# Kernel tuning notes

Measured on AMD Instinct MI355X. Metric: run time of the kernel, lower is better.

## Reference

```python
import jax, jax.numpy as jnp
import numpy as np

BN_EPS = 1e-5
SG = jax.lax.stop_gradient


def _silu(z):
    return z * jax.nn.sigmoid(z)


def _binary_activation(x):
    # forward value = sign(x); backward goes through piecewise quadratic out3 (STE)
    out1 = jnp.where(x < -1, -1.0, x * x + 2 * x)
    out2 = jnp.where(x < 0, out1, -x * x + 2 * x)
    out3 = jnp.where(x < 1, out2, 1.0)
    return SG(jnp.sign(x)) - SG(out3) + out3


def _binarize_weight(w):
    # per-output-channel scaling factor * sign(w), STE through clipped weights
    sf = SG(jnp.mean(jnp.abs(w), axis=(1, 2, 3), keepdims=True))  # [O,1,1,1]
    cw = jnp.clip(w, -1.0, 1.0)
    return SG(sf * jnp.sign(w)) - SG(cw) + cw


def _conv3x3_s2(x, w, b):
    y = jax.lax.conv_general_dilated(
        x, w, window_strides=(2, 2), padding=((1, 1), (1, 1)),
        dimension_numbers=("NCHW", "OIHW", "NCHW"))
    return y + b[None, :, None, None]


def _batchnorm_train(x, gamma, beta):
    # training-mode BN: batch statistics over (N,H,W), biased variance
    mean = jnp.mean(x, axis=(0, 2, 3), keepdims=True)
    var = jnp.mean((x - mean) ** 2, axis=(0, 2, 3), keepdims=True)
    xhat = (x - mean) * jax.lax.rsqrt(var + BN_EPS)
    return xhat * gamma[None, :, None, None] + beta[None, :, None, None]


def _learnable_bias(x, emb, w, b):
    # bias = zero_module(linear)(SiLU(emb)) broadcast over H,W
    bias = _silu(emb) @ w.T + b  # [B, C]
    return x + bias[:, :, None, None]


def _avgpool2(x):
    B, C, H, W = x.shape
    return x.reshape(B, C, H // 2, 2, W // 2, 2).mean(axis=(3, 5))


def setup_inputs() -> dict:
    key = jax.random.key(0)
    ks = jax.random.split(key, 16)
    B, Cin, P, E, H, W = 32, 128, 256, 512, 64, 64
    scalor = P // Cin  # 2
    inp = {
        "x": jax.random.normal(ks[0], (B, Cin, H, W), jnp.float32),
        "emb": jax.random.normal(ks[1], (B, E), jnp.float32),
        "m1_w": jax.random.normal(ks[2], (Cin, E), jnp.float32) * 0.02,
        "m1_b": jnp.zeros((Cin,), jnp.float32),
        "conv_w": jax.random.uniform(ks[3], (scalor, Cin, Cin, 3, 3), jnp.float32, -1.0, 1.0) * 0.1,
        "conv_b": jax.random.normal(ks[4], (scalor, Cin), jnp.float32) * 0.01,
        "bn_g": jnp.ones((scalor, Cin), jnp.float32),
        "bn_b": jnp.zeros((scalor, Cin), jnp.float32),
        "m2_w": jax.random.normal(ks[5], (P, E), jnp.float32) * 0.02,
        "m2_b": jnp.zeros((P,), jnp.float32),
        "prelu_a": jnp.full((P,), 0.25, jnp.float32),
        "m3_w": jax.random.normal(ks[6], (P, E), jnp.float32) * 0.02,
        "m3_b": jnp.zeros((P,), jnp.float32),
    }
    return inp


def reference(x, emb, m1_w, m1_b, conv_w, conv_b, bn_g, bn_b,
              m2_w, m2_b, prelu_a, m3_w, m3_b):
    scalor = conv_w.shape[0]
    out = _learnable_bias(x, emb, m1_w, m1_b)
    out = _binary_activation(out)
    xp = _avgpool2(x)  # residual, [B,Cin,H/2,W/2]
    out_list = []
    for i in range(scalor):
        bw = _binarize_weight(conv_w[i])
        y = _conv3x3_s2(out, bw, conv_b[i])
        y = _batchnorm_train(y, bn_g[i], bn_b[i])
        out_list.append(y + xp)
    o = jnp.concatenate(out_list, axis=1)  # [B, planes, H/2, W/2]
    o = _learnable_bias(o, emb, m2_w, m2_b)
    a = prelu_a[None, :, None, None]
    o = jnp.where(o > 0, o, a * o)  # PReLU per channel
    o = _learnable_bias(o, emb, m3_w, m3_b)
    return o
```

## Files before the change

### kernel.cpp

```cpp
#include <hip/hip_runtime.h>
#include <cstdint>
#include <cstddef>

#define B_  32
#define CIN 128
#define P_  256
#define E_  512
#define H_  64
#define W_  64
#define HO  32
#define WO  32

#define APITCH 65
#define APIX   4225

__global__ void k_bw(const float* __restrict__ emb,
                     const float* __restrict__ m1_w, const float* __restrict__ m1_b,
                     const float* __restrict__ m2_w, const float* __restrict__ m2_b,
                     const float* __restrict__ m3_w, const float* __restrict__ m3_b,
                     const float* __restrict__ conv_w,
                     float* __restrict__ b1, float* __restrict__ b2, float* __restrict__ b3,
                     float* __restrict__ sf, unsigned int* __restrict__ wbits,
                     int* __restrict__ cwrow, int* __restrict__ cwcol, int* __restrict__ cw0,
                     float* __restrict__ s1, float* __restrict__ s2) {
    int bid = blockIdx.x;
    int tid = threadIdx.x;
    int wave = tid >> 6, lane = tid & 63;

    if (bid < B_ * 160) {
        int n = bid / 160, rg = bid % 160;
        int row = rg * 4 + wave;
        const float* sp = emb + n * E_;
        const float* wrow; float bias; float* dst;
        if (row < CIN)            { wrow = m1_w + (size_t)row * E_;          bias = m1_b[row]; dst = b1 + n * CIN + row; }
        else if (row < CIN + P_)  { int c = row - CIN;      wrow = m2_w + (size_t)c * E_; bias = m2_b[c]; dst = b2 + n * P_ + c; }
        else                      { int c = row - CIN - P_; wrow = m3_w + (size_t)c * E_; bias = m3_b[c]; dst = b3 + n * P_ + c; }
        float acc = 0.f;
        #pragma unroll
        for (int j = 0; j < 8; j++) {
            int k = j * 64 + lane;
            float e = sp[k];
            acc += (e / (1.f + expf(-e))) * wrow[k];
        }
        #pragma unroll
        for (int off = 32; off > 0; off >>= 1) acc += __shfl_down(acc, off);
        if (lane == 0) *dst = acc + bias;
        return;
    }

    int base = (bid - B_ * 160) * 2;
    int oc = base + (wave >> 1);
    int iw = wave & 1;
    int i  = iw * 64 + lane;
    if (lane == 0 && iw == 0) { s1[oc] = 0.f; s2[oc] = 0.f; }
    const float* wp = conv_w + ((size_t)oc * CIN + i) * 9;
    float w[9]; float s = 0.f;
    int pc[9];
    #pragma unroll
    for (int t = 0; t < 9; t++) { w[t] = wp[t]; s += fabsf(w[t]); }
    #pragma unroll
    for (int t = 0; t < 9; t++) {
        unsigned long long m = __ballot(w[t] < 0.f);
        pc[t] = __popcll(m);
        if (lane == 0) {
            wbits[oc * 36 + t * 4 + iw * 2 + 0] = (unsigned int)(m & 0xffffffffull);
            wbits[oc * 36 + t * 4 + iw * 2 + 1] = (unsigned int)(m >> 32);
        }
    }
    #pragma unroll
    for (int off = 32; off > 0; off >>= 1) s += __shfl_down(s, off);
    __shared__ float sred[4];
    __shared__ int spc[4][9];
    if (lane == 0) {
        sred[wave] = s;
        #pragma unroll
        for (int t = 0; t < 9; t++) spc[wave][t] = pc[t];
    }
    __syncthreads();
    if (tid == 0) {
        sf[base] = (sred[0] + sred[1]) / 1152.f;
        int c_[9];
        #pragma unroll
        for (int t = 0; t < 9; t++) c_[t] = spc[0][t] + spc[1][t];
        cwrow[base] = 384 - 2 * (c_[0] + c_[1] + c_[2]);
        cwcol[base] = 384 - 2 * (c_[0] + c_[3] + c_[6]);
        cw0[base]   = 128 - 2 * c_[0];
    } else if (tid == 128) {
        sf[base + 1] = (sred[2] + sred[3]) / 1152.f;
        int c_[9];
        #pragma unroll
        for (int t = 0; t < 9; t++) c_[t] = spc[2][t] + spc[3][t];
        cwrow[base + 1] = 384 - 2 * (c_[0] + c_[1] + c_[2]);
        cwcol[base + 1] = 384 - 2 * (c_[0] + c_[3] + c_[6]);
        cw0[base + 1]   = 128 - 2 * c_[0];
    }
}

__global__ void k_prep(const float* __restrict__ x, const float* __restrict__ b1,
                       unsigned int* __restrict__ abits, float* __restrict__ xpool) {
    __shared__ float sb1[CIN];
    int n = blockIdx.x >> 5, h2 = blockIdx.x & 31;
    int tid = threadIdx.x;
    for (int i = tid; i < CIN; i += 256) sb1[i] = b1[n * CIN + i];
    __syncthreads();

    if (h2 == 0) {
        for (int i = tid; i < 129; i += 256) {
            size_t idx = (i < 65) ? ((size_t)n * APIX + i)
                                  : ((size_t)n * APIX + (size_t)(i - 64) * APITCH);
            ((uint4*)abits)[idx] = make_uint4(0u, 0u, 0u, 0u);
        }
    }

    int wg = tid >> 6, lane = tid & 63;
    int w = lane, w2 = w >> 1;
    const float* xb = x + ((size_t)(n * CIN + wg * 32)) * (H_ * W_) + (size_t)(2 * h2) * W_ + w;
    float* xpq = xpool + ((size_t)(n * CIN + wg * 32)) * (HO * WO) + h2 * WO + w2;
    unsigned int mt = 0, mb = 0;
    #pragma unroll 8
    for (int j = 0; j < 32; j++) {
        float vt = xb[(size_t)j * (H_ * W_)];
        float vb = xb[(size_t)j * (H_ * W_) + W_];
        float bc = sb1[wg * 32 + j];
        mt |= (vt + bc < 0.f ? 1u : 0u) << j;
        mb |= (vb + bc < 0.f ? 1u : 0u) << j;
        float p = vt + vb;
        p += __shfl_xor(p, 1);
        if ((w & 1) == 0) xpq[(size_t)j * (HO * WO)] = 0.25f * p;
    }
    size_t basei = ((size_t)n * APIX + (size_t)(2 * h2 + 1) * APITCH + (w + 1)) * 4 + wg;
    abits[basei] = mt;
    abits[basei + APITCH * 4] = mb;
}

__global__ void __launch_bounds__(256, 6) k_conv(const unsigned int* __restrict__ abits,
                                                 const unsigned int* __restrict__ wbits,
                                                 const int* __restrict__ cwrow,
                                                 const int* __restrict__ cwcol,
                                                 const int* __restrict__ cw0,
                                                 short* __restrict__ y16) {
    int bid = blockIdx.x;
    int strip = bid & 3, og = (bid >> 2) & 15, n = bid >> 6;
    int tid = threadIdx.x;
    int oh = strip * 8 + (tid >> 5), ow = tid & 31;
    bool r0 = (oh == 0), c0 = (ow == 0);
    bool rc0 = r0 && c0;

    const uint4* asrc = ((const uint4*)abits) + (size_t)n * APIX;
    uint4 img[9];
    #pragma unroll
    for (int kh = 0; kh < 3; kh++) {
        #pragma unroll
        for (int kw = 0; kw < 3; kw++) {
            img[kh * 3 + kw] = asrc[(2 * oh + kh) * APITCH + (2 * ow + kw)];
        }
    }
    #pragma unroll
    for (int t = 0; t < 9; t++) {
        asm volatile("" : "+v"(img[t].x), "+v"(img[t].y), "+v"(img[t].z), "+v"(img[t].w));
    }

    int ocb = og * 16;
    const uint4* wp = ((const uint4*)wbits) + (size_t)ocb * 9;
    short* yp = y16 + (((size_t)n * P_ + ocb) << 10) + strip * 256 + tid;
    #pragma unroll 4
    for (int o = 0; o < 16; o++) {
        int popsum = 0;
        #pragma unroll
        for (int t = 0; t < 9; t++) {
            uint4 a = img[t];
            uint4 w = wp[o * 9 + t];
            popsum += __popc(a.x ^ w.x) + __popc(a.y ^ w.y) +
                      __popc(a.z ^ w.z) + __popc(a.w ^ w.w);
        }
        int corr = (r0 ? cwrow[ocb + o] : 0) + (c0 ? cwcol[ocb + o] : 0) - (rc0 ? cw0[ocb + o] : 0);
        int s = 1152 - 2 * popsum - corr;
        yp[(size_t)o << 10] = (short)s;
    }
}

__global__ void k_stat(const short* __restrict__ y16,
                       float* __restrict__ s1, float* __restrict__ s2) {
    int oc = blockIdx.x & 255, nq = blockIdx.x >> 8;
    int tid = threadIdx.x;
    int acc = 0, acc2 = 0;
    #pragma unroll
    for (int k = 0; k < 8; k++) {
        int n = nq * 8 + k;
        short4 v = ((const short4*)(y16 + (((size_t)n * P_ + oc) << 10)))[tid];
        int a0 = v.x, a1 = v.y, a2 = v.z, a3 = v.w;
        acc  += a0 + a1 + a2 + a3;
        acc2 += a0 * a0 + a1 * a1 + a2 * a2 + a3 * a3;
    }
    float f1 = (float)acc, f2 = (float)acc2;
    #pragma unroll
    for (int off = 32; off > 0; off >>= 1) { f1 += __shfl_down(f1, off); f2 += __shfl_down(f2, off); }
    __shared__ float r1[4], r2[4];
    int wave = tid >> 6, lane = tid & 63;
    if (lane == 0) { r1[wave] = f1; r2[wave] = f2; }
    __syncthreads();
    if (tid == 0)       atomicAdd(s1 + oc, r1[0] + r1[1] + r1[2] + r1[3]);
    else if (tid == 64) atomicAdd(s2 + oc, r2[0] + r2[1] + r2[2] + r2[3]);
}

__global__ void k_epi(const short* __restrict__ y16, const float* __restrict__ xpool,
                      const float* __restrict__ sf,
                      const float* __restrict__ s1, const float* __restrict__ s2,
                      const float* __restrict__ bn_g, const float* __restrict__ bn_b,
                      const float* __restrict__ b2, const float* __restrict__ b3,
                      const float* __restrict__ prelu_a, float* __restrict__ out) {
    int i4 = blockIdx.x * blockDim.x + threadIdx.x;
    int pix4 = i4 & 255;
    int c = (i4 >> 8) & 255;
    int n = i4 >> 16;
    short4 yv = ((const short4*)y16)[i4];
    float4 xv = ((const float4*)xpool)[((n * CIN + (c & 127)) << 8) + pix4];
    const float inv = 1.f / (B_ * HO * WO);
    float sc = sf[c];
    float m = sc * s1[c] * inv;
    float var = fmaf(-m, m, sc * sc * s2[c] * inv);
    float r = rsqrtf(var + 1e-5f) * bn_g[c];
    float add0 = bn_b[c] + b2[n * P_ + c];
    float a = prelu_a[c];
    float b3v = b3[n * P_ + c];
    float o0 = (sc * (float)yv.x - m) * r + add0 + xv.x; o0 = (o0 > 0.f ? o0 : a * o0) + b3v;
    float o1 = (sc * (float)yv.y - m) * r + add0 + xv.y; o1 = (o1 > 0.f ? o1 : a * o1) + b3v;
    float o2 = (sc * (float)yv.z - m) * r + add0 + xv.z; o2 = (o2 > 0.f ? o2 : a * o2) + b3v;
    float o3 = (sc * (float)yv.w - m) * r + add0 + xv.w; o3 = (o3 > 0.f ? o3 : a * o3) + b3v;
    ((float4*)out)[i4] = make_float4(o0, o1, o2, o3);
}

extern "C" void kernel_launch(void* const* d_in, const int* in_sizes, int n_in,
                              void* d_out, int out_size, void* d_ws, size_t ws_size,
                              hipStream_t stream) {
    const float* x      = (const float*)d_in[0];
    const float* emb    = (const float*)d_in[1];
    const float* m1_w   = (const float*)d_in[2];
    const float* m1_b   = (const float*)d_in[3];
    const float* conv_w = (const float*)d_in[4];
    const float* bn_g   = (const float*)d_in[6];
    const float* bn_b   = (const float*)d_in[7];
    const float* m2_w   = (const float*)d_in[8];
    const float* m2_b   = (const float*)d_in[9];
    const float* prelu_a= (const float*)d_in[10];
    const float* m3_w   = (const float*)d_in[11];
    const float* m3_b   = (const float*)d_in[12];

    float* out = (float*)d_out;

    float* wsf = (float*)d_ws;
    float* b1    = wsf;
    float* b2    = wsf + 4096;
    float* b3    = wsf + 12288;
    float* sf    = wsf + 20480;
    float* s1    = wsf + 20736;
    float* s2    = wsf + 20992;
    unsigned int* wbits = (unsigned int*)(wsf + 21248);
    int* cwrow = (int*)(wsf + 30464);
    int* cwcol = (int*)(wsf + 30720);
    int* cw0   = (int*)(wsf + 30976);
    unsigned int* abits = (unsigned int*)(wsf + 31232);
    float* xpool = wsf + 572032;
    short* y16   = (short*)(wsf + 4766336);

    k_bw   <<<B_ * 160 + P_ / 2, 256, 0, stream>>>(emb, m1_w, m1_b, m2_w, m2_b, m3_w, m3_b,
                                                   conv_w, b1, b2, b3, sf, wbits,
                                                   cwrow, cwcol, cw0, s1, s2);
    k_prep <<<B_ * 32, 256, 0, stream>>>(x, b1, abits, xpool);
    k_conv <<<B_ * 64, 256, 0, stream>>>(abits, wbits, cwrow, cwcol, cw0, y16);
    k_stat <<<4 * P_, 256, 0, stream>>>(y16, s1, s2);
    k_epi  <<<(B_ * P_ * HO * WO) / (4 * 256), 256, 0, stream>>>(y16, xpool, sf, s1, s2,
                                                                 bn_g, bn_b, b2, b3, prelu_a, out);
}
```

Before: 188.7 us.

## Fuse prep, conv, stats and epilogue into one cooperative kernel

Merges the prep, binary conv, batch-statistics and epilogue kernels into one cooperative kernel with two grid-wide syncs. Conv outputs stay in LDS instead of round-tripping an int16 buffer through global memory, and the per-channel sums are reduced in-block before atomics. Each block now handles 32 output channels over 1024 blocks. This drops the separate stats pass and the global y buffer, but costs grid-sync overhead, higher LDS use that caps occupancy, and stride-1024 per-channel scalar stores in the epilogue instead of float4 stores.

After: 404.5 us. 2.14x slower.

```diff
diff --git a/kernel.cpp b/kernel.cpp
--- a/kernel.cpp
+++ b/kernel.cpp
@@ -1,6 +1,9 @@
 #include <hip/hip_runtime.h>
+#include <hip/hip_cooperative_groups.h>
 #include <cstdint>
 #include <cstddef>
+
+namespace cg = cooperative_groups;
 
 #define B_  32
 #define CIN 128
@@ -96,52 +99,62 @@
     }
 }
 
-__global__ void k_prep(const float* __restrict__ x, const float* __restrict__ b1,
-                       unsigned int* __restrict__ abits, float* __restrict__ xpool) {
+__global__ void __launch_bounds__(256, 4)
+k_fused(const float* __restrict__ x, const float* __restrict__ b1,
+        const unsigned int* __restrict__ wbits,
+        const int* __restrict__ cwrow, const int* __restrict__ cwcol, const int* __restrict__ cw0,
+        const float* __restrict__ sf, float* __restrict__ s1, float* __restrict__ s2,
+        const float* __restrict__ bn_g, const float* __restrict__ bn_b,
+        const float* __restrict__ b2, const float* __restrict__ b3,
+        const float* __restrict__ prelu_a,
+        unsigned int* __restrict__ abits, float* __restrict__ xpool, float* __restrict__ out) {
+    cg::grid_group grid = cg::this_grid();
     __shared__ float sb1[CIN];
-    int n = blockIdx.x >> 5, h2 = blockIdx.x & 31;
+    __shared__ short y_lds[32][256];
+    __shared__ int red1[32][33], red2[32][33];
+
+    int bid = blockIdx.x;
     int tid = threadIdx.x;
-    for (int i = tid; i < CIN; i += 256) sb1[i] = b1[n * CIN + i];
-    __syncthreads();
-
-    if (h2 == 0) {
-        for (int i = tid; i < 129; i += 256) {
-            size_t idx = (i < 65) ? ((size_t)n * APIX + i)
-                                  : ((size_t)n * APIX + (size_t)(i - 64) * APITCH);
-            ((uint4*)abits)[idx] = make_uint4(0u, 0u, 0u, 0u);
-        }
-    }
-
-    int wg = tid >> 6, lane = tid & 63;
-    int w = lane, w2 = w >> 1;
-    const float* xb = x + ((size_t)(n * CIN + wg * 32)) * (H_ * W_) + (size_t)(2 * h2) * W_ + w;
-    float* xpq = xpool + ((size_t)(n * CIN + wg * 32)) * (HO * WO) + h2 * WO + w2;
-    unsigned int mt = 0, mb = 0;
-    #pragma unroll 8
-    for (int j = 0; j < 32; j++) {
-        float vt = xb[(size_t)j * (H_ * W_)];
-        float vb = xb[(size_t)j * (H_ * W_) + W_];
-        float bc = sb1[wg * 32 + j];
-        mt |= (vt + bc < 0.f ? 1u : 0u) << j;
-        mb |= (vb + bc < 0.f ? 1u : 0u) << j;
-        float p = vt + vb;
-        p += __shfl_xor(p, 1);
-        if ((w & 1) == 0) xpq[(size_t)j * (HO * WO)] = 0.25f * p;
-    }
-    size_t basei = ((size_t)n * APIX + (size_t)(2 * h2 + 1) * APITCH + (w + 1)) * 4 + wg;
-    abits[basei] = mt;
-    abits[basei + APITCH * 4] = mb;
-}
-
-__global__ void __launch_bounds__(256, 6) k_conv(const unsigned int* __restrict__ abits,
-                                                 const unsigned int* __restrict__ wbits,
-                                                 const int* __restrict__ cwrow,
-                                                 const int* __restrict__ cwcol,
-                                                 const int* __restrict__ cw0,
-                                                 short* __restrict__ y16) {
-    int bid = blockIdx.x;
-    int strip = bid & 3, og = (bid >> 2) & 15, n = bid >> 6;
-    int tid = threadIdx.x;
+    int n = bid >> 5;
+    int wave = tid >> 6, lane = tid & 63;
+
+    {
+        int h2 = bid & 31;
+        for (int i = tid; i < CIN; i += 256) sb1[i] = b1[n * CIN + i];
+        __syncthreads();
+
+        if (h2 == 0) {
+            for (int i = tid; i < 129; i += 256) {
+                size_t idx = (i < 65) ? ((size_t)n * APIX + i)
+                                      : ((size_t)n * APIX + (size_t)(i - 64) * APITCH);
+                ((uint4*)abits)[idx] = make_uint4(0u, 0u, 0u, 0u);
+            }
+        }
+
+        int wg = wave;
+        int w = lane, w2 = w >> 1;
+        const float* xb = x + ((size_t)(n * CIN + wg * 32)) * (H_ * W_) + (size_t)(2 * h2) * W_ + w;
+        float* xpq = xpool + ((size_t)(n * CIN + wg * 32)) * (HO * WO) + h2 * WO + w2;
+        unsigned int mt = 0, mb = 0;
+        #pragma unroll 8
+        for (int j = 0; j < 32; j++) {
+            float vt = xb[(size_t)j * (H_ * W_)];
+            float vb = xb[(size_t)j * (H_ * W_) + W_];
+            float bc = sb1[wg * 32 + j];
+            mt |= (vt + bc < 0.f ? 1u : 0u) << j;
+            mb |= (vb + bc < 0.f ? 1u : 0u) << j;
+            float p = vt + vb;
+            p += __shfl_xor(p, 1);
+            if ((w & 1) == 0) xpq[(size_t)j * (HO * WO)] = 0.25f * p;
+        }
+        size_t basei = ((size_t)n * APIX + (size_t)(2 * h2 + 1) * APITCH + (w + 1)) * 4 + wg;
+        abits[basei] = mt;
+        abits[basei + APITCH * 4] = mb;
+    }
+    grid.sync();
+
+    int strip = bid & 3, ocg = (bid >> 2) & 7;
+    int ocb = ocg * 32;
     int oh = strip * 8 + (tid >> 5), ow = tid & 31;
     bool r0 = (oh == 0), c0 = (ow == 0);
     bool rc0 = r0 && c0;
@@ -160,11 +173,9 @@
         asm volatile("" : "+v"(img[t].x), "+v"(img[t].y), "+v"(img[t].z), "+v"(img[t].w));
     }
 
-    int ocb = og * 16;
     const uint4* wp = ((const uint4*)wbits) + (size_t)ocb * 9;
-    short* yp = y16 + (((size_t)n * P_ + ocb) << 10) + strip * 256 + tid;
     #pragma unroll 4
-    for (int o = 0; o < 16; o++) {
+    for (int o = 0; o < 32; o++) {
         int popsum = 0;
         #pragma unroll
         for (int t = 0; t < 9; t++) {
@@ -175,59 +186,49 @@
         }
         int corr = (r0 ? cwrow[ocb + o] : 0) + (c0 ? cwcol[ocb + o] : 0) - (rc0 ? cw0[ocb + o] : 0);
         int s = 1152 - 2 * popsum - corr;
-        yp[(size_t)o << 10] = (short)s;
-    }
-}
-
-__global__ void k_stat(const short* __restrict__ y16,
-                       float* __restrict__ s1, float* __restrict__ s2) {
-    int oc = blockIdx.x & 255, nq = blockIdx.x >> 8;
-    int tid = threadIdx.x;
-    int acc = 0, acc2 = 0;
-    #pragma unroll
-    for (int k = 0; k < 8; k++) {
-        int n = nq * 8 + k;
-        short4 v = ((const short4*)(y16 + (((size_t)n * P_ + oc) << 10)))[tid];
-        int a0 = v.x, a1 = v.y, a2 = v.z, a3 = v.w;
-        acc  += a0 + a1 + a2 + a3;
-        acc2 += a0 * a0 + a1 * a1 + a2 * a2 + a3 * a3;
-    }
-    float f1 = (float)acc, f2 = (float)acc2;
-    #pragma unroll
-    for (int off = 32; off > 0; off >>= 1) { f1 += __shfl_down(f1, off); f2 += __shfl_down(f2, off); }
-    __shared__ float r1[4], r2[4];
-    int wave = tid >> 6, lane = tid & 63;
-    if (lane == 0) { r1[wave] = f1; r2[wave] = f2; }
+        y_lds[o][tid] = (short)s;
+        int vs = s, v2 = s * s;
+        vs += __shfl_down(vs, 32); v2 += __shfl_down(v2, 32);
+        vs += __shfl_down(vs, 16); v2 += __shfl_down(v2, 16);
+        vs += __shfl_down(vs, 8);  v2 += __shfl_down(v2, 8);
+        if (lane < 8) { red1[o][wave * 8 + lane] = vs; red2[o][wave * 8 + lane] = v2; }
+    }
     __syncthreads();
-    if (tid == 0)       atomicAdd(s1 + oc, r1[0] + r1[1] + r1[2] + r1[3]);
-    else if (tid == 64) atomicAdd(s2 + oc, r2[0] + r2[1] + r2[2] + r2[3]);
-}
-
-__global__ void k_epi(const short* __restrict__ y16, const float* __restrict__ xpool,
-                      const float* __restrict__ sf,
-                      const float* __restrict__ s1, const float* __restrict__ s2,
-                      const float* __restrict__ bn_g, const float* __restrict__ bn_b,
-                      const float* __restrict__ b2, const float* __restrict__ b3,
-                      const float* __restrict__ prelu_a, float* __restrict__ out) {
-    int i4 = blockIdx.x * blockDim.x + threadIdx.x;
-    int pix4 = i4 & 255;
-    int c = (i4 >> 8) & 255;
-    int n = i4 >> 16;
-    short4 yv = ((const short4*)y16)[i4];
-    float4 xv = ((const float4*)xpool)[((n * CIN + (c & 127)) << 8) + pix4];
-    const float inv = 1.f / (B_ * HO * WO);
-    float sc = sf[c];
-    float m = sc * s1[c] * inv;
-    float var = fmaf(-m, m, sc * sc * s2[c] * inv);
-    float r = rsqrtf(var + 1e-5f) * bn_g[c];
-    float add0 = bn_b[c] + b2[n * P_ + c];
-    float a = prelu_a[c];
-    float b3v = b3[n * P_ + c];
-    float o0 = (sc * (float)yv.x - m) * r + add0 + xv.x; o0 = (o0 > 0.f ? o0 : a * o0) + b3v;
-    float o1 = (sc * (float)yv.y - m) * r + add0 + xv.y; o1 = (o1 > 0.f ? o1 : a * o1) + b3v;
-    float o2 = (sc * (float)yv.z - m) * r + add0 + xv.z; o2 = (o2 > 0.f ? o2 : a * o2) + b3v;
-    float o3 = (sc * (float)yv.w - m) * r + add0 + xv.w; o3 = (o3 > 0.f ? o3 : a * o3) + b3v;
-    ((float4*)out)[i4] = make_float4(o0, o1, o2, o3);
+    if (tid < 64) {
+        int o = tid & 31;
+        int a = 0;
+        if (tid < 32) {
+            #pragma unroll
+            for (int p = 0; p < 32; p++) a += red1[o][p];
+            atomicAdd(s1 + ocb + o, (float)a);
+        } else {
+            #pragma unroll
+            for (int p = 0; p < 32; p++) a += red2[o][p];
+            atomicAdd(s2 + ocb + o, (float)a);
+        }
+    }
+    grid.sync();
+
+    {
+        const float inv = 1.f / (B_ * HO * WO);
+        int pixoff = strip * 256 + tid;
+        #pragma unroll 4
+        for (int o = 0; o < 32; o++) {
+            int c = ocb + o;
+            float sc = sf[c];
+            float m = sc * s1[c] * inv;
+            float var = fmaf(-m, m, sc * sc * s2[c] * inv);
+            float r = rsqrtf(var + 1e-5f) * bn_g[c];
+            float add0 = bn_b[c] + b2[n * P_ + c];
+            float aP = prelu_a[c];
+            float b3v = b3[n * P_ + c];
+            float yv = (float)y_lds[o][tid];
+            float xv = xpool[(((size_t)n * CIN + (c & 127)) << 10) + pixoff];
+            float o0 = (sc * yv - m) * r + add0 + xv;
+            o0 = (o0 > 0.f ? o0 : aP * o0) + b3v;
+            out[(((size_t)n * P_ + c) << 10) + pixoff] = o0;
+        }
+    }
 }
 
 extern "C" void kernel_launch(void* const* d_in, const int* in_sizes, int n_in,
@@ -261,14 +262,28 @@
     int* cw0   = (int*)(wsf + 30976);
     unsigned int* abits = (unsigned int*)(wsf + 31232);
     float* xpool = wsf + 572032;
-    short* y16   = (short*)(wsf + 4766336);
-
-    k_bw   <<<B_ * 160 + P_ / 2, 256, 0, stream>>>(emb, m1_w, m1_b, m2_w, m2_b, m3_w, m3_b,
-                                                   conv_w, b1, b2, b3, sf, wbits,
-                                                   cwrow, cwcol, cw0, s1, s2);
-    k_prep <<<B_ * 32, 256, 0, stream>>>(x, b1, abits, xpool);
-    k_conv <<<B_ * 64, 256, 0, stream>>>(abits, wbits, cwrow, cwcol, cw0, y16);
-    k_stat <<<4 * P_, 256, 0, stream>>>(y16, s1, s2);
-    k_epi  <<<(B_ * P_ * HO * WO) / (4 * 256), 256, 0, stream>>>(y16, xpool, sf, s1, s2,
-                                                                 bn_g, bn_b, b2, b3, prelu_a, out);
+
+    k_bw <<<B_ * 160 + P_ / 2, 256, 0, stream>>>(emb, m1_w, m1_b, m2_w, m2_b, m3_w, m3_b,
+                                                 conv_w, b1, b2, b3, sf, wbits,
+                                                 cwrow, cwcol, cw0, s1, s2);
+
+    void* kargs[17];
+    kargs[0]  = (void*)&x;
+    kargs[1]  = (void*)&b1;
+    kargs[2]  = (void*)&wbits;
+    kargs[3]  = (void*)&cwrow;
+    kargs[4]  = (void*)&cwcol;
+    kargs[5]  = (void*)&cw0;
+    kargs[6]  = (void*)&sf;
+    kargs[7]  = (void*)&s1;
+    kargs[8]  = (void*)&s2;
+    kargs[9]  = (void*)&bn_g;
+    kargs[10] = (void*)&bn_b;
+    kargs[11] = (void*)&b2;
+    kargs[12] = (void*)&b3;
+    kargs[13] = (void*)&prelu_a;
+    kargs[14] = (void*)&abits;
+    kargs[15] = (void*)&xpool;
+    kargs[16] = (void*)&out;
+    hipLaunchCooperativeKernel((void*)k_fused, dim3(B_ * 32), dim3(256), kargs, 0, stream);
 }
```
